# Kernel tuning notes

Hardware: AMD Instinct MI355X
Metric: run time of the kernel (lower is better)

Reference implementation:

```python
import jax, jax.numpy as jnp
import numpy as np

NUM_HEADS = 16
EPS = 1e-12  # torch F.normalize default eps


def _l2norm(t):
    n = jnp.linalg.norm(t, axis=-1, keepdims=True)
    return t / jnp.maximum(n, EPS)


def setup_inputs() -> dict:
    key = jax.random.key(0)
    ks = jax.random.split(key, 5)
    N, C, d = 16, 1024, 1024
    x = jax.random.normal(ks[0], (N, C, d), dtype=jnp.float32)
    Wq = jax.random.normal(ks[1], (d, d), dtype=jnp.float32) * 0.02
    Wk = jax.random.normal(ks[2], (d, d), dtype=jnp.float32) * 0.02
    Wv = jax.random.normal(ks[3], (d, d), dtype=jnp.float32) * 0.02
    Wo = jax.random.normal(ks[4], (d, d), dtype=jnp.float32) * 0.02
    norm_const = 0.5 * jnp.ones((1, NUM_HEADS, 1, 1), dtype=jnp.float32)
    return {"x": x, "Wq": Wq, "Wk": Wk, "Wv": Wv, "Wo": Wo, "norm_const": norm_const}


def reference(x, Wq, Wk, Wv, Wo, norm_const):
    # attn_type='cosine', causal=False branch of Attention.forward
    N, C, d = x.shape
    H = NUM_HEADS
    hd = d // H
    # torch nn.Linear(bias=False): y = x @ W.T ; split heads -> [N, H, C, hd]
    def proj(W):
        return (x @ W.T).reshape(N, C, H, hd).transpose(0, 2, 1, 3)
    q = _l2norm(proj(Wq))
    k = _l2norm(proj(Wk))
    v = proj(Wv)
    # values = values / C ** sigmoid(norm_const)  (per-head scalar)
    v = v / jnp.power(jnp.float32(C), jax.nn.sigmoid(norm_const))
    # linear-attention reordering: q @ (k^T @ v); kv is [N, H, hd, hd]
    kv = jnp.einsum('nhcd,nhce->nhde', k, v)
    attn = jnp.einsum('nhcd,nhde->nhce', q, kv)
    out = attn.transpose(0, 2, 1, 3).reshape(N, C, d)
    return out @ Wo.T
```

## Files before the change

kernel.cpp:

```cpp
#include <hip/hip_runtime.h>
#include <stdint.h>

typedef __attribute__((ext_vector_type(4))) float f32x4;
typedef __attribute__((ext_vector_type(8))) short bf16x8;
typedef __attribute__((ext_vector_type(4))) unsigned short u16x4;
typedef __attribute__((ext_vector_type(4))) unsigned int u32x4;

typedef __attribute__((address_space(3))) char lds_t;
typedef const __attribute__((address_space(1))) char gmem_t;

__device__ __forceinline__ float bf2f(unsigned short u) {
  union { unsigned int u; float f; } a; a.u = ((unsigned int)u) << 16; return a.f;
}
__device__ __forceinline__ unsigned short f2bf(float f) {
  union { float f; unsigned int u; } a; a.f = f;
  unsigned int r = a.u + 0x7fffu + ((a.u >> 16) & 1u);
  return (unsigned short)(r >> 16);
}

__global__ __launch_bounds__(256) void cvt_all(
    const float* __restrict__ x, const float* __restrict__ W0, const float* __restrict__ W1,
    const float* __restrict__ W2, const float* __restrict__ W3,
    unsigned short* __restrict__ xb, unsigned short* __restrict__ wqkv,
    unsigned short* __restrict__ wob)
{
  const int b = blockIdx.x;
  const float* src;
  unsigned short* dst;
  int i;
  if (b < 8192) {
    src = x; dst = xb; i = b * 2048 + threadIdx.x * 8;
  } else {
    const int s = (b - 8192) >> 9;
    const int bb = (b - 8192) & 511;
    i = bb * 2048 + threadIdx.x * 8;
    src = (s == 0) ? W0 : (s == 1) ? W1 : (s == 2) ? W2 : W3;
    dst = (s < 3) ? (wqkv + s * 1048576) : wob;
  }
  const f32x4 a = *(const f32x4*)(src + i);
  const f32x4 c = *(const f32x4*)(src + i + 4);
  alignas(16) unsigned short o[8];
#pragma unroll
  for (int k = 0; k < 4; ++k) { o[k] = f2bf(a[k]); o[4 + k] = f2bf(c[k]); }
  *(u32x4*)(dst + i) = *(const u32x4*)o;
}

template<int GX, int MODE>
__global__ __launch_bounds__(512, 2) void gemm256(
    const unsigned short* __restrict__ A, const unsigned short* __restrict__ B,
    void* __restrict__ O0, void* __restrict__ O1, void* __restrict__ O2,
    const float* __restrict__ nc)
{
  constexpr int K = 1024;
  constexpr int NT = K / 64;
  constexpr int NWG = GX * 64;
  constexpr int CPX = NWG >> 3;
  const int p = blockIdx.y * GX + blockIdx.x;
  const int lid = (p & 7) * CPX + (p >> 3);
  const int bm0 = (lid / GX) * 256;
  const int bn0 = (lid % GX) * 256;
  const int t = threadIdx.x;
  const int l = t & 63;
  const int w = t >> 6;
  const int wm = w >> 2;
  const int wn = w & 3;

  __shared__ char smem[131072];

  const int srow = t >> 3;
  const int schunk = t & 7;
  const int sck = schunk ^ (srow & 7);

#define STAGE_A(so_, kt_, lam_)                                                                  \
  __builtin_amdgcn_global_load_lds(                                                             \
      (gmem_t*)(A + (long long)(bm0 + (lam_) * 64 + srow) * K + (kt_) * 64 + sck * 8),          \
      (lds_t*)(smem + (so_) + ((lam_) * 64 + srow) * 128 + schunk * 16), 16, 0, 0)
#define STAGE_B(so_, kt_, lam_)                                                                  \
  __builtin_amdgcn_global_load_lds(                                                             \
      (gmem_t*)(B + (long long)(bn0 + (lam_) * 64 + srow) * K + (kt_) * 64 + sck * 8),          \
      (lds_t*)(smem + (so_) + 32768 + ((lam_) * 64 + srow) * 128 + schunk * 16), 16, 0, 0)

  const int xr = l & 7;
  const int chalf = l >> 4;
  int aoff[8], boff[4];
#pragma unroll
  for (int fr = 0; fr < 8; ++fr) aoff[fr] = (wm * 128 + fr * 16 + (l & 15)) * 128;
#pragma unroll
  for (int fc = 0; fc < 4; ++fc) boff[fc] = 32768 + (wn * 64 + fc * 16 + (l & 15)) * 128;

  f32x4 acc[8][4];
#pragma unroll
  for (int i = 0; i < 8; ++i)
#pragma unroll
    for (int j = 0; j < 4; ++j) acc[i][j] = f32x4{0.f, 0.f, 0.f, 0.f};

#pragma unroll
  for (int lam = 0; lam < 4; ++lam) STAGE_A(0, 0, lam);
#pragma unroll
  for (int lam = 0; lam < 4; ++lam) STAGE_B(0, 0, lam);
#pragma unroll
  for (int lam = 0; lam < 4; ++lam) STAGE_B(65536, 1, lam);
  asm volatile("s_waitcnt vmcnt(4)" ::: "memory");
  __builtin_amdgcn_s_barrier();
  __builtin_amdgcn_sched_barrier(0);

  for (int u = 0; u < NT; ++u) {
    const int slot = (u & 1) << 16;
    const int nslot = slot ^ 65536;
    bf16x8 bv[4][2];
#pragma unroll
    for (int q = 0; q < 4; ++q) {
      if (q == 0) {
#pragma unroll
        for (int j = 0; j < 4; ++j)
#pragma unroll
          for (int ks = 0; ks < 2; ++ks)
            bv[j][ks] = *(const bf16x8*)(smem + slot + boff[j] + (((ks * 4 + chalf) ^ xr) * 16));
      }
      bf16x8 av[2][2];
#pragma unroll
      for (int d = 0; d < 2; ++d)
#pragma unroll
        for (int ks = 0; ks < 2; ++ks)
          av[d][ks] = *(const bf16x8*)(smem + slot + aoff[2 * q + d] + (((ks * 4 + chalf) ^ xr) * 16));
      if (q == 0)      { if (u + 1 < NT) { STAGE_A(nslot, u + 1, 0); STAGE_A(nslot, u + 1, 1); } }
      else if (q == 1) { if (u + 1 < NT) { STAGE_A(nslot, u + 1, 2); STAGE_A(nslot, u + 1, 3); } }
      else if (q == 2) { if (u + 2 < NT) { STAGE_B(slot, u + 2, 0);  STAGE_B(slot, u + 2, 1); } }
      else             { if (u + 2 < NT) { STAGE_B(slot, u + 2, 2);  STAGE_B(slot, u + 2, 3); } }
      __builtin_amdgcn_s_barrier();
      asm volatile("s_waitcnt lgkmcnt(0)" ::: "memory");
      __builtin_amdgcn_sched_barrier(0);
      __builtin_amdgcn_s_setprio(1);
#pragma unroll
      for (int d = 0; d < 2; ++d)
#pragma unroll
        for (int j = 0; j < 4; ++j)
#pragma unroll
          for (int ks = 0; ks < 2; ++ks)
            acc[2 * q + d][j] =
                __builtin_amdgcn_mfma_f32_16x16x32_bf16(av[d][ks], bv[j][ks], acc[2 * q + d][j], 0, 0, 0);
      __builtin_amdgcn_s_setprio(0);
      if (q == 3) {
        if (u + 2 < NT) { asm volatile("s_waitcnt vmcnt(4)" ::: "memory"); }
        else            { asm volatile("s_waitcnt vmcnt(0)" ::: "memory"); }
      }
      __builtin_amdgcn_s_barrier();
      __builtin_amdgcn_sched_barrier(0);
    }
  }
#undef STAGE_A
#undef STAGE_B

  const int wcol0 = bn0 + wn * 64;
  const int rowb = bm0 + wm * 128 + (l >> 4) * 4;

  if (MODE == 0) {
    float* Op = (float*)O0;
    const int colb = wcol0 + (l & 15);
#pragma unroll
    for (int i = 0; i < 8; ++i)
#pragma unroll
      for (int j = 0; j < 4; ++j)
#pragma unroll
        for (int r = 0; r < 4; ++r)
          Op[(long long)(rowb + i * 16 + r) * 1024 + (colb + j * 16)] = acc[i][j][r];
  } else {
    const int sel = wcol0 >> 10;
    const int col_in = wcol0 & 1023;
    const int h = col_in >> 6;
    if (sel < 2) {
#pragma unroll
      for (int i = 0; i < 8; ++i)
#pragma unroll
        for (int r = 0; r < 4; ++r) {
          float s = 0.f;
#pragma unroll
          for (int j = 0; j < 4; ++j) s += acc[i][j][r] * acc[i][j][r];
          s += __shfl_xor(s, 1); s += __shfl_xor(s, 2);
          s += __shfl_xor(s, 4); s += __shfl_xor(s, 8);
          const float inv = 1.f / fmaxf(sqrtf(s), 1e-12f);
#pragma unroll
          for (int j = 0; j < 4; ++j) acc[i][j][r] *= inv;
        }
    } else {
      const float sig = 1.f / (1.f + expf(-nc[h]));
      const float vsc = expf(-6.9314718055994530942f * sig);
#pragma unroll
      for (int i = 0; i < 8; ++i)
#pragma unroll
        for (int j = 0; j < 4; ++j)
#pragma unroll
          for (int r = 0; r < 4; ++r) acc[i][j][r] *= vsc;
    }
    if (sel == 0) {
      unsigned short* Op = (unsigned short*)O0;
      const int colb = col_in + (l & 15);
#pragma unroll
      for (int i = 0; i < 8; ++i)
#pragma unroll
        for (int j = 0; j < 4; ++j)
#pragma unroll
          for (int r = 0; r < 4; ++r)
            Op[(long long)(rowb + i * 16 + r) * 1024 + (colb + j * 16)] = f2bf(acc[i][j][r]);
    } else {
      unsigned short* Tp = (unsigned short*)(sel == 1 ? O1 : O2)
                         + ((long long)((bm0 >> 10) * 16 + h) * 64) * 1024;
      const int c0 = (bm0 & 1023) + wm * 128 + (l >> 4) * 4;
#pragma unroll
      for (int j = 0; j < 4; ++j) {
        const long long drow = (long long)(j * 16 + (l & 15)) * 1024;
#pragma unroll
        for (int i = 0; i < 8; ++i) {
          u16x4 o;
#pragma unroll
          for (int r = 0; r < 4; ++r) o[r] = f2bf(acc[i][j][r]);
          *(u16x4*)(Tp + drow + c0 + i * 16) = o;
        }
      }
    }
  }
}

__global__ __launch_bounds__(256) void kv_mfma(
    const unsigned short* __restrict__ vT, const unsigned short* __restrict__ kT,
    unsigned short* __restrict__ kvT)
{
  const int h = blockIdx.x, n = blockIdx.y;
  const int t = threadIdx.x, l = t & 63, w = t >> 6;
  __shared__ char smem[131072];
  const long long base = (long long)(n * 16 + h) * 64 * 1024;
  const int srow = l >> 3;
  const int schunk = l & 7;
  char* wbuf = smem + w * 32768;

#define KV_STAGE(buf_, cc_) do {                                                                  \
    const int col_ = w * 256 + (cc_) * 64;                                                        \
    _Pragma("unroll")                                                                             \
    for (int i_ = 0; i_ < 8; ++i_) {                                                              \
      const int r_ = i_ * 8 + srow;                                                               \
      const int sc_ = schunk ^ srow;                                                              \
      __builtin_amdgcn_global_load_lds((gmem_t*)(vT + base + (long long)r_ * 1024 + col_ + sc_ * 8), \
                                       (lds_t*)((buf_) + r_ * 128 + schunk * 16), 16, 0, 0);      \
      __builtin_amdgcn_global_load_lds((gmem_t*)(kT + base + (long long)r_ * 1024 + col_ + sc_ * 8), \
                                       (lds_t*)((buf_) + 8192 + r_ * 128 + schunk * 16), 16, 0, 0); \
    }                                                                                             \
  } while (0)

  const int xr = l & 7, chalf = l >> 4;
  f32x4 acc[4][4];
#pragma unroll
  for (int i = 0; i < 4; ++i)
#pragma unroll
    for (int j = 0; j < 4; ++j) acc[i][j] = f32x4{0.f, 0.f, 0.f, 0.f};

  KV_STAGE(wbuf, 0);
  for (int cc = 0; cc < 4; ++cc) {
    char* cur = wbuf + (cc & 1) * 16384;
    if (cc < 3) {
      KV_STAGE(wbuf + ((cc + 1) & 1) * 16384, cc + 1);
      asm volatile("s_waitcnt vmcnt(16)" ::: "memory");
    } else {
      asm volatile("s_waitcnt vmcnt(0)" ::: "memory");
    }
    bf16x8 av[4][2], bvv[4][2];
#pragma unroll
    for (int m = 0; m < 4; ++m)
#pragma unroll
      for (int ks = 0; ks < 2; ++ks) {
        const int ch = ((ks * 4 + chalf) ^ xr) * 16;
        av[m][ks]  = *(const bf16x8*)(cur + (m * 16 + (l & 15)) * 128 + ch);
        bvv[m][ks] = *(const bf16x8*)(cur + 8192 + (m * 16 + (l & 15)) * 128 + ch);
      }
#pragma unroll
    for (int m = 0; m < 4; ++m)
#pragma unroll
      for (int j = 0; j < 4; ++j)
#pragma unroll
        for (int ks = 0; ks < 2; ++ks)
          acc[m][j] = __builtin_amdgcn_mfma_f32_16x16x32_bf16(av[m][ks], bvv[j][ks], acc[m][j], 0, 0, 0);
  }
#undef KV_STAGE

  __syncthreads();
  float* red = (float*)smem;
#pragma unroll
  for (int m = 0; m < 4; ++m)
#pragma unroll
    for (int j = 0; j < 4; ++j)
      *(f32x4*)&red[w * 4096 + (m * 4 + j) * 256 + l * 4] = acc[m][j];
  __syncthreads();

  const int e = t >> 2, d0 = (t & 3) * 16;
  const int m = e >> 4, rr = e & 3, lhi = (e & 15) >> 2;
  alignas(16) unsigned short o16[16];
#pragma unroll
  for (int dd = 0; dd < 16; ++dd) {
    const int d = d0 + dd;
    const int f = m * 4 + (d >> 4);
    const int pos = (lhi * 16 + (d & 15)) * 4 + rr;
    float s = red[f * 256 + pos] + red[4096 + f * 256 + pos] +
              red[8192 + f * 256 + pos] + red[12288 + f * 256 + pos];
    o16[dd] = f2bf(s);
  }
  unsigned short* dst = kvT + (long long)(n * 16 + h) * 4096 + e * 64 + d0;
  *(u32x4*)dst = *(const u32x4*)&o16[0];
  *((u32x4*)dst + 1) = *(const u32x4*)&o16[8];
}

__global__ __launch_bounds__(256) void attn_mfma(
    unsigned short* __restrict__ q, const unsigned short* __restrict__ kvT)
{
  const int ct = blockIdx.x, h = blockIdx.y, n = blockIdx.z;
  const int t = threadIdx.x, l = t & 63, w = t >> 6;
  __shared__ char smem[40960];
  const long long R0 = (long long)n * 1024 + ct * 256;
  {
    const int sr = t >> 3;
    const int sc = (t & 7) ^ (sr & 7);
#pragma unroll
    for (int i = 0; i < 8; ++i) {
      const int r = i * 32 + sr;
      __builtin_amdgcn_global_load_lds((gmem_t*)(q + (R0 + r) * 1024 + h * 64 + sc * 8),
                                       (lds_t*)(smem + r * 128 + (t & 7) * 16), 16, 0, 0);
    }
#pragma unroll
    for (int i = 0; i < 2; ++i) {
      const int r = i * 32 + sr;
      __builtin_amdgcn_global_load_lds((gmem_t*)(kvT + (long long)(n * 16 + h) * 4096 + r * 64 + sc * 8),
                                       (lds_t*)(smem + 32768 + r * 128 + (t & 7) * 16), 16, 0, 0);
    }
  }
  asm volatile("s_waitcnt vmcnt(0)" ::: "memory");
  __syncthreads();

  const int xr = l & 7, chalf = l >> 4;
  f32x4 acc[4][4];
#pragma unroll
  for (int i = 0; i < 4; ++i)
#pragma unroll
    for (int j = 0; j < 4; ++j) acc[i][j] = f32x4{0.f, 0.f, 0.f, 0.f};
  bf16x8 av[4][2], bvv[4][2];
#pragma unroll
  for (int m = 0; m < 4; ++m)
#pragma unroll
    for (int ks = 0; ks < 2; ++ks) {
      const int ch = ((ks * 4 + chalf) ^ xr) * 16;
      av[m][ks]  = *(const bf16x8*)(smem + (w * 64 + m * 16 + (l & 15)) * 128 + ch);
      bvv[m][ks] = *(const bf16x8*)(smem + 32768 + (m * 16 + (l & 15)) * 128 + ch);
    }
#pragma unroll
  for (int m = 0; m < 4; ++m)
#pragma unroll
    for (int j = 0; j < 4; ++j)
#pragma unroll
      for (int ks = 0; ks < 2; ++ks)
        acc[m][j] = __builtin_amdgcn_mfma_f32_16x16x32_bf16(av[m][ks], bvv[j][ks], acc[m][j], 0, 0, 0);

  const int rb = w * 64 + (l >> 4) * 4;
#pragma unroll
  for (int m = 0; m < 4; ++m)
#pragma unroll
    for (int j = 0; j < 4; ++j)
#pragma unroll
      for (int r = 0; r < 4; ++r)
        q[(R0 + rb + m * 16 + r) * 1024 + h * 64 + j * 16 + (l & 15)] = f2bf(acc[m][j][r]);
}

extern "C" void kernel_launch(void* const* d_in, const int* in_sizes, int n_in,
                              void* d_out, int out_size, void* d_ws, size_t ws_size,
                              hipStream_t stream) {
  (void)in_sizes; (void)n_in; (void)out_size; (void)ws_size;
  const float* x  = (const float*)d_in[0];
  const float* Wq = (const float*)d_in[1];
  const float* Wk = (const float*)d_in[2];
  const float* Wv = (const float*)d_in[3];
  const float* Wo = (const float*)d_in[4];
  const float* nc = (const float*)d_in[5];

  unsigned short* xb  = (unsigned short*)d_out;
  unsigned short* kvT = (unsigned short*)((char*)d_out + 33554432ll);

  char* ws = (char*)d_ws;
  unsigned short* wqkv = (unsigned short*)ws;
  unsigned short* wob  = wqkv + 3 * 1048576;
  unsigned short* qb   = wob + 1048576;
  unsigned short* kTb  = qb + 16777216;
  unsigned short* vTb  = kTb + 16777216;

  cvt_all<<<10240, 256, 0, stream>>>(x, Wq, Wk, Wv, Wo, xb, wqkv, wob);

  gemm256<12, 1><<<dim3(12, 64), 512, 0, stream>>>(xb, wqkv, qb, kTb, vTb, nc);
  kv_mfma<<<dim3(16, 16), 256, 0, stream>>>(vTb, kTb, kvT);
  attn_mfma<<<dim3(4, 16, 16), 256, 0, stream>>>(qb, kvT);
  gemm256<4, 0><<<dim3(4, 64), 512, 0, stream>>>(qb, wob, d_out, nullptr, nullptr, nullptr);
}
```

Measured before the change: 214.4 us.

## Store K/V in blocked 4-row interleaved layout for contiguous kv loads

The projection GEMM now writes K and V per head in a blocked layout: groups of 4 sequence positions, each holding a 64-dim x 4 tile. Each wave in the GEMM epilogue then writes one contiguous 2KB region, and the kv kernel's global-to-LDS staging becomes fully linear with no XOR swizzle. MFMA operands are assembled from two 8-byte LDS reads 512 bytes apart, replacing a single swizzled 16-byte read. This trades more, smaller LDS reads, with possible bank conflicts, for coalesced global writes and loads.

```diff
diff --git a/kernel.cpp b/kernel.cpp
--- a/kernel.cpp
+++ b/kernel.cpp
@@ -16,6 +16,12 @@
   union { float f; unsigned int u; } a; a.f = f;
   unsigned int r = a.u + 0x7fffu + ((a.u >> 16) & 1u);
   return (unsigned short)(r >> 16);
+}
+__device__ __forceinline__ bf16x8 ld_pair512(const char* p) {
+  union { bf16x8 v; u16x4 h[2]; } u;
+  u.h[0] = *(const u16x4*)p;
+  u.h[1] = *(const u16x4*)(p + 512);
+  return u.v;
 }
 
 __global__ __launch_bounds__(256) void cvt_all(
@@ -204,17 +210,17 @@
             Op[(long long)(rowb + i * 16 + r) * 1024 + (colb + j * 16)] = f2bf(acc[i][j][r]);
     } else {
       unsigned short* Tp = (unsigned short*)(sel == 1 ? O1 : O2)
-                         + ((long long)((bm0 >> 10) * 16 + h) * 64) * 1024;
-      const int c0 = (bm0 & 1023) + wm * 128 + (l >> 4) * 4;
+                         + (long long)((bm0 >> 10) * 16 + h) * 65536;
+      const int cbase = (bm0 & 1023) + wm * 128 + (l >> 4) * 4;
 #pragma unroll
       for (int j = 0; j < 4; ++j) {
-        const long long drow = (long long)(j * 16 + (l & 15)) * 1024;
+        const int dbase4 = (j * 16 + (l & 15)) * 4;
 #pragma unroll
         for (int i = 0; i < 8; ++i) {
           u16x4 o;
 #pragma unroll
           for (int r = 0; r < 4; ++r) o[r] = f2bf(acc[i][j][r]);
-          *(u16x4*)(Tp + drow + c0 + i * 16) = o;
+          *(u16x4*)(Tp + (long long)((cbase >> 2) + i * 4) * 256 + dbase4) = o;
         }
       }
     }
@@ -222,31 +228,27 @@
 }
 
 __global__ __launch_bounds__(256) void kv_mfma(
-    const unsigned short* __restrict__ vT, const unsigned short* __restrict__ kT,
+    const unsigned short* __restrict__ vL, const unsigned short* __restrict__ kL,
     unsigned short* __restrict__ kvT)
 {
   const int h = blockIdx.x, n = blockIdx.y;
   const int t = threadIdx.x, l = t & 63, w = t >> 6;
   __shared__ char smem[131072];
-  const long long base = (long long)(n * 16 + h) * 64 * 1024;
-  const int srow = l >> 3;
-  const int schunk = l & 7;
+  const long long base = (long long)(n * 16 + h) * 65536;
   char* wbuf = smem + w * 32768;
 
 #define KV_STAGE(buf_, cc_) do {                                                                  \
-    const int col_ = w * 256 + (cc_) * 64;                                                        \
+    const long long s0 = base + (long long)(w * 64 + (cc_) * 16) * 256;                          \
     _Pragma("unroll")                                                                             \
     for (int i_ = 0; i_ < 8; ++i_) {                                                              \
-      const int r_ = i_ * 8 + srow;                                                               \
-      const int sc_ = schunk ^ srow;                                                              \
-      __builtin_amdgcn_global_load_lds((gmem_t*)(vT + base + (long long)r_ * 1024 + col_ + sc_ * 8), \
-                                       (lds_t*)((buf_) + r_ * 128 + schunk * 16), 16, 0, 0);      \
-      __builtin_amdgcn_global_load_lds((gmem_t*)(kT + base + (long long)r_ * 1024 + col_ + sc_ * 8), \
-                                       (lds_t*)((buf_) + 8192 + r_ * 128 + schunk * 16), 16, 0, 0); \
+      __builtin_amdgcn_global_load_lds((gmem_t*)(vL + s0 + i_ * 512 + l * 8),                     \
+                                       (lds_t*)((buf_) + i_ * 1024 + l * 16), 16, 0, 0);          \
+      __builtin_amdgcn_global_load_lds((gmem_t*)(kL + s0 + i_ * 512 + l * 8),                     \
+                                       (lds_t*)((buf_) + 8192 + i_ * 1024 + l * 16), 16, 0, 0);   \
     }                                                                                             \
   } while (0)
 
-  const int xr = l & 7, chalf = l >> 4;
+  const int chalf = l >> 4;
   f32x4 acc[4][4];
 #pragma unroll
   for (int i = 0; i < 4; ++i)
@@ -267,9 +269,9 @@
     for (int m = 0; m < 4; ++m)
 #pragma unroll
       for (int ks = 0; ks < 2; ++ks) {
-        const int ch = ((ks * 4 + chalf) ^ xr) * 16;
-        av[m][ks]  = *(const bf16x8*)(cur + (m * 16 + (l & 15)) * 128 + ch);
-        bvv[m][ks] = *(const bf16x8*)(cur + 8192 + (m * 16 + (l & 15)) * 128 + ch);
+        const int a0 = (ks * 4 + chalf) * 1024 + (m * 16 + (l & 15)) * 8;
+        av[m][ks]  = ld_pair512(cur + a0);
+        bvv[m][ks] = ld_pair512(cur + 8192 + a0);
       }
 #pragma unroll
     for (int m = 0; m < 4; ++m)
@@ -384,13 +386,13 @@
   unsigned short* wqkv = (unsigned short*)ws;
   unsigned short* wob  = wqkv + 3 * 1048576;
   unsigned short* qb   = wob + 1048576;
-  unsigned short* kTb  = qb + 16777216;
-  unsigned short* vTb  = kTb + 16777216;
+  unsigned short* kLb  = qb + 16777216;
+  unsigned short* vLb  = kLb + 16777216;
 
   cvt_all<<<10240, 256, 0, stream>>>(x, Wq, Wk, Wv, Wo, xb, wqkv, wob);
 
-  gemm256<12, 1><<<dim3(12, 64), 512, 0, stream>>>(xb, wqkv, qb, kTb, vTb, nc);
-  kv_mfma<<<dim3(16, 16), 256, 0, stream>>>(vTb, kTb, kvT);
+  gemm256<12, 1><<<dim3(12, 64), 512, 0, stream>>>(xb, wqkv, qb, kLb, vLb, nc);
+  kv_mfma<<<dim3(16, 16), 256, 0, stream>>>(vLb, kLb, kvT);
   attn_mfma<<<dim3(4, 16, 16), 256, 0, stream>>>(qb, kvT);
   gemm256<4, 0><<<dim3(4, 64), 512, 0, stream>>>(qb, wob, d_out, nullptr, nullptr, nullptr);
 }
```

Measured after the change: 200.8 us. -6.3%, faster.
